# Kernel optimization log

Measured on AMD Instinct MI355X. Metric: run time of the kernel, lower is better.

The kernel has to match this reference:

```python
import jax, jax.numpy as jnp
import numpy as np

B, P, ENC = 128, 625, 512
A, E, H, V = 256, 256, 512, 70
START_TOK, END_TOK = 68, 69


def setup_inputs() -> dict:
    key = jax.random.key(0)
    ks = jax.random.split(key, 20)
    w = lambda k, shape: jax.random.normal(k, shape, jnp.float32) * 0.02
    return {
        "encoder_out": jax.random.normal(ks[0], (B, P, ENC), jnp.float32),
        "emb": w(ks[1], (V, E)),
        "We": w(ks[2], (ENC, A)), "be": jnp.zeros((A,), jnp.float32),
        "Wd": w(ks[3], (H, A)),   "bd": jnp.zeros((A,), jnp.float32),
        "wf": w(ks[4], (A,)),     "bf": jnp.zeros((), jnp.float32),
        "Wh0": w(ks[5], (ENC, H)), "bh0": jnp.zeros((H,), jnp.float32),
        "Wc0": w(ks[6], (ENC, H)), "bc0": jnp.zeros((H,), jnp.float32),
        "Wb": w(ks[7], (H, ENC)), "bb": jnp.zeros((ENC,), jnp.float32),
        "Wih": w(ks[8], (E + ENC, 4 * H)), "Whh": w(ks[9], (H, 4 * H)),
        "bih": jnp.zeros((4 * H,), jnp.float32), "bhh": jnp.zeros((4 * H,), jnp.float32),
        "Wfc": w(ks[10], (H, V)), "bfc": jnp.zeros((V,), jnp.float32),
        "decode_lengths": 70,
    }


def _decode(encoder_out, emb, We, be, Wd, bd, wf, bf, Wh0, bh0, Wc0, bc0,
            Wb, bb, Wih, Whh, bih, bhh, Wfc, bfc, decode_lengths):
    enc = encoder_out  # [B, P, ENC]
    batch = enc.shape[0]
    # encoder_att projection is constant across timesteps -> hoist out of loop
    att1 = enc @ We + be                      # [B, P, A]
    mean_enc = enc.mean(axis=1)               # [B, ENC]
    h0 = mean_enc @ Wh0 + bh0                 # [B, H]
    c0 = mean_enc @ Wc0 + bc0                 # [B, H]
    emb0 = emb[jnp.full((batch,), START_TOK)]  # [B, E]
    lstm_b = bih + bhh

    def step(carry, _):
        h, c, emb_t, done = carry
        att2 = h @ Wd + bd                                            # [B, A]
        e = jnp.einsum('bpa,a->bp', jax.nn.relu(att1 + att2[:, None, :]), wf) + bf
        alpha = jax.nn.softmax(e, axis=1)                             # [B, P]
        awe = jnp.einsum('bp,bpe->be', alpha, enc)                    # [B, ENC]
        awe = jax.nn.sigmoid(h @ Wb + bb) * awe                       # gated
        gates = jnp.concatenate([emb_t, awe], axis=1) @ Wih + h @ Whh + lstm_b
        i_, f_, g_, o_ = jnp.split(gates, 4, axis=1)                  # torch order i,f,g,o
        c_new = jax.nn.sigmoid(f_) * c + jax.nn.sigmoid(i_) * jnp.tanh(g_)
        h_new = jax.nn.sigmoid(o_) * jnp.tanh(c_new)
        preds = h_new @ Wfc + bfc                                     # [B, V] (dropout eval = id)
        preds_out = jnp.where(done, 0.0, preds)                       # zeros after early break
        done_new = done | (jnp.argmax(preds) == END_TOK)              # flat argmax, as in torch
        emb_new = emb[jnp.argmax(preds, axis=-1)]                     # greedy feedback
        return (h_new, c_new, emb_new, done_new), preds_out

    init = (h0, c0, emb0, jnp.array(False))
    _, preds_seq = jax.lax.scan(step, init, None, length=decode_lengths)
    return jnp.transpose(preds_seq, (1, 0, 2))  # [B, T, V]


def reference(encoder_out, emb, We, be, Wd, bd, wf, bf, Wh0, bh0, Wc0, bc0,
              Wb, bb, Wih, Whh, bih, bhh, Wfc, bfc, decode_lengths):
    return _decode(encoder_out, emb, We, be, Wd, bd, wf, bf, Wh0, bh0, Wc0, bc0,
                   Wb, bb, Wih, Whh, bih, bhh, Wfc, bfc, decode_lengths)
```

## Files before the change

### kernel.cpp

```cpp
#include <hip/hip_runtime.h>
#include <math.h>

#define Bn 128
#define Pn 625
#define ENCn 512
#define An 256
#define En 256
#define Hn 512
#define Vn 70
#define G4n 2048
#define STARTT 68
#define ENDT 69
#define NCHUNK 5
#define PCH 125
#define PSTRIDE 520
#define KSPLIT 16
#define KCH 80


__global__ __launch_bounds__(256) void k_mean(const float* __restrict__ enc,
                                              float* __restrict__ mean_enc) {
  int b = blockIdx.x, t = threadIdx.x;
  const float* e = enc + (size_t)b * Pn * ENCn;
  float s0 = 0.f, s1 = 0.f;
  for (int p = 0; p < Pn; ++p) {
    s0 += e[(size_t)p * ENCn + t];
    s1 += e[(size_t)p * ENCn + t + 256];
  }
  mean_enc[b * ENCn + t] = s0 * (1.0f / 625.0f);
  mean_enc[b * ENCn + t + 256] = s1 * (1.0f / 625.0f);
}

__global__ __launch_bounds__(512) void k_init(const float* __restrict__ mean_enc,
                       const float* __restrict__ Wh0, const float* __restrict__ bh0,
                       const float* __restrict__ Wc0, const float* __restrict__ bc0,
                       const float* __restrict__ emb,
                       float* __restrict__ h0, float* __restrict__ c0,
                       float* __restrict__ emb_t, int* __restrict__ done_arr) {
  int b = blockIdx.x, t = threadIdx.x;
  const float* W = blockIdx.y ? Wc0 : Wh0;
  const float* bias = blockIdx.y ? bc0 : bh0;
  float* out = blockIdx.y ? c0 : h0;
  __shared__ float ms[ENCn];
  ms[t] = mean_enc[b * ENCn + t];
  __syncthreads();
  float s = bias[t];
  for (int k = 0; k < ENCn; ++k) s += ms[k] * W[k * Hn + t];
  out[b * Hn + t] = s;
  if (blockIdx.y == 0 && t < En) emb_t[b * En + t] = emb[STARTT * En + t];
  if (blockIdx.y == 0 && b == 0 && t == 0) done_arr[0] = 0;
}

__global__ __launch_bounds__(256) void k_att1(const float* __restrict__ Am,
                       const float* __restrict__ We,
                       const float* __restrict__ be, float* __restrict__ att1) {
  __shared__ float sA[16][128];
  __shared__ float sB[16][128];
  int n0 = blockIdx.x * 128, m0 = blockIdx.y * 128;
  int t = threadIdx.x;
  int tm = (t >> 4) * 8, tn = (t & 15) * 8;
  float acc[8][8];
#pragma unroll
  for (int i = 0; i < 8; ++i)
#pragma unroll
    for (int j = 0; j < 8; ++j) acc[i][j] = 0.f;
  for (int k0 = 0; k0 < 512; k0 += 16) {
    __syncthreads();
#pragma unroll
    for (int i = 0; i < 8; ++i) {
      int idx = t + i * 256;
      int mm = idx >> 4, kk = idx & 15;
      sA[kk][mm] = Am[(size_t)(m0 + mm) * 512 + k0 + kk];
      int kk2 = idx >> 7, nn = idx & 127;
      sB[kk2][nn] = We[(size_t)(k0 + kk2) * 256 + n0 + nn];
    }
    __syncthreads();
#pragma unroll
    for (int kk = 0; kk < 16; ++kk) {
      float a[8], bq[8];
      *(float4*)&a[0] = *(const float4*)&sA[kk][tm];
      *(float4*)&a[4] = *(const float4*)&sA[kk][tm + 4];
      *(float4*)&bq[0] = *(const float4*)&sB[kk][tn];
      *(float4*)&bq[4] = *(const float4*)&sB[kk][tn + 4];
#pragma unroll
      for (int i = 0; i < 8; ++i)
#pragma unroll
        for (int j = 0; j < 8; ++j) acc[i][j] += a[i] * bq[j];
    }
  }
  float ber[8];
  *(float4*)&ber[0] = *(const float4*)&be[n0 + tn];
  *(float4*)&ber[4] = *(const float4*)&be[n0 + tn + 4];
#pragma unroll
  for (int i = 0; i < 8; ++i) {
    float o[8];
#pragma unroll
    for (int j = 0; j < 8; ++j) o[j] = acc[i][j] + ber[j];
    *(float4*)&att1[(size_t)(m0 + tm + i) * An + n0 + tn] = *(float4*)&o[0];
    *(float4*)&att1[(size_t)(m0 + tm + i) * An + n0 + tn + 4] = *(float4*)&o[4];
  }
}


__global__ __launch_bounds__(256) void k_proj(const float* __restrict__ h,
                       const float* __restrict__ Wd, const float* __restrict__ bd,
                       const float* __restrict__ Wb, const float* __restrict__ bbv,
                       float* __restrict__ att2, float* __restrict__ gate,
                       const float* __restrict__ preds,
                       const int* __restrict__ done_prev, int* __restrict__ done_cur,
                       int do_flat) {
  int t = threadIdx.x;
  if (blockIdx.x == Bn) {
    if (!do_flat) return;
    __shared__ float sv[256];
    __shared__ int si[256];
    float bv = -1e30f; int bi = 0x7fffffff;
    for (int i = t; i < Bn * Vn; i += 256) {
      float v = preds[i];
      if (v > bv) { bv = v; bi = i; }
    }
    sv[t] = bv; si[t] = bi;
    __syncthreads();
    for (int s = 128; s > 0; s >>= 1) {
      if (t < s) {
        if (sv[t + s] > sv[t] || (sv[t + s] == sv[t] && si[t + s] < si[t])) {
          sv[t] = sv[t + s]; si[t] = si[t + s];
        }
      }
      __syncthreads();
    }
    if (t == 0) *done_cur = (*done_prev) | (si[0] == ENDT ? 1 : 0);
    return;
  }
  int b = blockIdx.x;
  __shared__ float hsh[Hn];
  hsh[t] = h[b * Hn + t];
  hsh[t + 256] = h[b * Hn + t + 256];
  __syncthreads();
  float s0 = bd[t];
  float s1 = bbv[t], s2 = bbv[t + 256];
  for (int k = 0; k < Hn; ++k) {
    float hv = hsh[k];
    s0 += hv * Wd[(size_t)k * An + t];
    s1 += hv * Wb[(size_t)k * ENCn + t];
    s2 += hv * Wb[(size_t)k * ENCn + t + 256];
  }
  att2[b * An + t] = s0;
  gate[b * ENCn + t] = 1.f / (1.f + expf(-s1));
  gate[b * ENCn + t + 256] = 1.f / (1.f + expf(-s2));
}

__global__ __launch_bounds__(256) void k_attn(const float* __restrict__ att1,
                       const float* __restrict__ att2,
                       const float* __restrict__ wf, const float* __restrict__ bfp,
                       const float* __restrict__ enc, float* __restrict__ part) {
  int c = blockIdx.x, b = blockIdx.y, t = threadIdx.x;
  int lane = t & 63, wv = t >> 6;
  int p0 = c * PCH;
  __shared__ float es[PCH];
  __shared__ float red[256];
  float4 a2 = ((const float4*)(att2 + b * An))[lane];
  float4 wfr = ((const float4*)wf)[lane];
  float bfv = *bfp;
  const float* a1b = att1 + ((size_t)b * Pn + p0) * An;
  for (int p = wv; p < PCH; p += 4) {
    float4 v = ((const float4*)(a1b + (size_t)p * An))[lane];
    float s = fmaxf(v.x + a2.x, 0.f) * wfr.x
            + fmaxf(v.y + a2.y, 0.f) * wfr.y
            + fmaxf(v.z + a2.z, 0.f) * wfr.z
            + fmaxf(v.w + a2.w, 0.f) * wfr.w;
    for (int o = 32; o > 0; o >>= 1) s += __shfl_down(s, o, 64);
    if (lane == 0) es[p] = s + bfv;
  }
  __syncthreads();
  float m = -1e30f;
  for (int i = t; i < PCH; i += 256) m = fmaxf(m, es[i]);
  red[t] = m;
  __syncthreads();
  for (int s = 128; s > 0; s >>= 1) {
    if (t < s) red[t] = fmaxf(red[t], red[t + s]);
    __syncthreads();
  }
  m = red[0];
  __syncthreads();
  float lp = 0.f;
  for (int i = t; i < PCH; i += 256) {
    float e2 = expf(es[i] - m);
    es[i] = e2;
    lp += e2;
  }
  red[t] = lp;
  __syncthreads();
  for (int s = 128; s > 0; s >>= 1) {
    if (t < s) red[t] += red[t + s];
    __syncthreads();
  }
  float l = red[0];
  float acc0 = 0.f, acc1 = 0.f;
  const float* ebase = enc + ((size_t)b * Pn + p0) * ENCn;
  for (int p = 0; p < PCH; ++p) {
    float wp = es[p];
    acc0 += wp * ebase[(size_t)p * ENCn + t];
    acc1 += wp * ebase[(size_t)p * ENCn + t + 256];
  }
  float* pp = part + (size_t)(b * NCHUNK + c) * PSTRIDE;
  if (t == 0) { pp[0] = m; pp[1] = l; }
  pp[8 + t] = acc0;
  pp[8 + t + 256] = acc1;
}

__global__ __launch_bounds__(256) void k_combine(const float* __restrict__ part,
                       const float* __restrict__ gate, float* __restrict__ awe) {
  int b = blockIdx.x, t = threadIdx.x;
  const float* pb = part + (size_t)b * NCHUNK * PSTRIDE;
  float M = -1e30f;
#pragma unroll
  for (int c = 0; c < NCHUNK; ++c) M = fmaxf(M, pb[c * PSTRIDE]);
  float L = 0.f, sc[NCHUNK];
#pragma unroll
  for (int c = 0; c < NCHUNK; ++c) {
    float s = expf(pb[c * PSTRIDE] - M);
    sc[c] = s;
    L += s * pb[c * PSTRIDE + 1];
  }
  float inv = 1.f / L;
  float a0 = 0.f, a1 = 0.f;
#pragma unroll
  for (int c = 0; c < NCHUNK; ++c) {
    a0 += sc[c] * pb[c * PSTRIDE + 8 + t];
    a1 += sc[c] * pb[c * PSTRIDE + 8 + t + 256];
  }
  awe[b * ENCn + t] = a0 * inv * gate[b * ENCn + t];
  awe[b * ENCn + t + 256] = a1 * inv * gate[b * ENCn + t + 256];
}

__global__ __launch_bounds__(256) void k_gates(const float* __restrict__ embt,
                       const float* __restrict__ awe, const float* __restrict__ h,
                       const float* __restrict__ Wih, const float* __restrict__ Whh,
                       float* __restrict__ gp) {
  int n0 = blockIdx.x * 64;
  int sI = blockIdx.y;
  int k0 = sI * KCH;
  int t = threadIdx.x;
  int tc = t & 15, tg = t >> 4;
  int nc = n0 + tc * 4;
  float4 acc[8];
#pragma unroll
  for (int r = 0; r < 8; ++r) acc[r] = make_float4(0.f, 0.f, 0.f, 0.f);
  for (int kk = 0; kk < KCH; kk += 4) {
    int k = k0 + kk;
    const float* wbase = (k < 768) ? (Wih + (size_t)k * G4n + nc)
                                   : (Whh + (size_t)(k - 768) * G4n + nc);
    float4 w0 = *(const float4*)(wbase);
    float4 w1 = *(const float4*)(wbase + G4n);
    float4 w2 = *(const float4*)(wbase + 2 * G4n);
    float4 w3 = *(const float4*)(wbase + 3 * G4n);
#pragma unroll
    for (int r = 0; r < 8; ++r) {
      int row = tg * 8 + r;
      float4 xv;
      if (k < 256)      xv = *(const float4*)(embt + row * En + k);
      else if (k < 768) xv = *(const float4*)(awe + row * ENCn + (k - 256));
      else              xv = *(const float4*)(h + row * Hn + (k - 768));
      acc[r].x += xv.x * w0.x + xv.y * w1.x + xv.z * w2.x + xv.w * w3.x;
      acc[r].y += xv.x * w0.y + xv.y * w1.y + xv.z * w2.y + xv.w * w3.y;
      acc[r].z += xv.x * w0.z + xv.y * w1.z + xv.z * w2.z + xv.w * w3.z;
      acc[r].w += xv.x * w0.w + xv.y * w1.w + xv.z * w2.w + xv.w * w3.w;
    }
  }
#pragma unroll
  for (int r = 0; r < 8; ++r)
    *(float4*)(gp + ((size_t)sI * Bn + tg * 8 + r) * G4n + nc) = acc[r];
}

__global__ __launch_bounds__(512) void k_lstm(const float* __restrict__ gp,
                       const float* __restrict__ bih, const float* __restrict__ bhh,
                       const float* __restrict__ c_in, float* __restrict__ c_out,
                       float* __restrict__ h_out,
                       const float* __restrict__ Wfc, const float* __restrict__ bfc,
                       const float* __restrict__ emb, float* __restrict__ preds,
                       float* __restrict__ emb_next, float* __restrict__ out,
                       const int* __restrict__ done_t, int step, int T) {
  int b = blockIdx.x, t = threadIdx.x;
  float gi = bih[t] + bhh[t];
  float gf = bih[t + 512] + bhh[t + 512];
  float gg = bih[t + 1024] + bhh[t + 1024];
  float go = bih[t + 1536] + bhh[t + 1536];
  for (int s = 0; s < KSPLIT; ++s) {
    const float* row = gp + ((size_t)s * Bn + b) * G4n;
    gi += row[t];
    gf += row[t + 512];
    gg += row[t + 1024];
    go += row[t + 1536];
  }
  float cv = (1.f / (1.f + expf(-gf))) * c_in[b * Hn + t]
           + (1.f / (1.f + expf(-gi))) * tanhf(gg);
  float hv = (1.f / (1.f + expf(-go))) * tanhf(cv);
  c_out[b * Hn + t] = cv;
  h_out[b * Hn + t] = hv;
  __shared__ float hs[Hn];
  __shared__ float ps[Vn];
  __shared__ int tokS;
  hs[t] = hv;
  __syncthreads();
  int lane = t & 63, wvi = t >> 6;
  for (int v = wvi; v < Vn; v += 8) {
    float s = 0.f;
    for (int k = lane; k < Hn; k += 64) s += hs[k] * Wfc[(size_t)k * Vn + v];
    for (int o = 32; o > 0; o >>= 1) s += __shfl_down(s, o, 64);
    if (lane == 0) ps[v] = s + bfc[v];
  }
  __syncthreads();
  int done = *done_t;
  if (t < Vn) {
    float pv = ps[t];
    preds[b * Vn + t] = pv;
    out[((size_t)b * T + step) * Vn + t] = done ? 0.f : pv;
  }
  if (t == 0) {
    float bv = ps[0]; int bi = 0;
    for (int v = 1; v < Vn; ++v)
      if (ps[v] > bv) { bv = ps[v]; bi = v; }
    tokS = bi;
  }
  __syncthreads();
  if (t < En) emb_next[b * En + t] = emb[tokS * En + t];
}


extern "C" void kernel_launch(void* const* d_in, const int* in_sizes, int n_in,
                              void* d_out, int out_size, void* d_ws, size_t ws_size,
                              hipStream_t stream) {
  const float* enc = (const float*)d_in[0];
  const float* emb = (const float*)d_in[1];
  const float* We  = (const float*)d_in[2];
  const float* be  = (const float*)d_in[3];
  const float* Wd  = (const float*)d_in[4];
  const float* bd  = (const float*)d_in[5];
  const float* wf  = (const float*)d_in[6];
  const float* bf  = (const float*)d_in[7];
  const float* Wh0 = (const float*)d_in[8];
  const float* bh0 = (const float*)d_in[9];
  const float* Wc0 = (const float*)d_in[10];
  const float* bc0 = (const float*)d_in[11];
  const float* Wb  = (const float*)d_in[12];
  const float* bb  = (const float*)d_in[13];
  const float* Wih = (const float*)d_in[14];
  const float* Whh = (const float*)d_in[15];
  const float* bih = (const float*)d_in[16];
  const float* bhh = (const float*)d_in[17];
  const float* Wfc = (const float*)d_in[18];
  const float* bfc = (const float*)d_in[19];
  int T = out_size / (Bn * Vn);

  float* w = (float*)d_ws;
  size_t off = 0;
  float* att1 = w + off;     off += (size_t)Bn * Pn * An;
  float* mean_enc = w + off; off += Bn * ENCn;
  float* hb0 = w + off;      off += Bn * Hn;
  float* hb1 = w + off;      off += Bn * Hn;
  float* cb0 = w + off;      off += Bn * Hn;
  float* cb1 = w + off;      off += Bn * Hn;
  float* eb0 = w + off;      off += Bn * En;
  float* eb1 = w + off;      off += Bn * En;
  float* att2 = w + off;     off += Bn * An;
  float* gate = w + off;     off += Bn * ENCn;
  float* part = w + off;     off += (size_t)Bn * NCHUNK * PSTRIDE;
  float* awe = w + off;      off += Bn * ENCn;
  float* gatesP = w + off;   off += (size_t)KSPLIT * Bn * G4n;
  float* preds = w + off;    off += Bn * Vn;
  off = (off + 255) & ~(size_t)255;
  int* done_arr = (int*)(w + off);

  float* hbuf[2] = {hb0, hb1};
  float* cbuf[2] = {cb0, cb1};
  float* ebuf[2] = {eb0, eb1};

  k_mean<<<Bn, 256, 0, stream>>>(enc, mean_enc);
  k_init<<<dim3(Bn, 2), 512, 0, stream>>>(mean_enc, Wh0, bh0, Wc0, bc0, emb,
                                          hb0, cb0, eb0, done_arr);
  k_att1<<<dim3(2, 625), 256, 0, stream>>>(enc, We, be, att1);

  int cur = 0;
  for (int t = 0; t < T; ++t) {
    int nxt = cur ^ 1;
    k_proj<<<Bn + 1, 256, 0, stream>>>(hbuf[cur], Wd, bd, Wb, bb, att2, gate, preds,
                                       done_arr + (t > 0 ? t - 1 : 0), done_arr + t,
                                       t > 0 ? 1 : 0);
    k_attn<<<dim3(NCHUNK, Bn), 256, 0, stream>>>(att1, att2, wf, bf, enc, part);
    k_combine<<<Bn, 256, 0, stream>>>(part, gate, awe);
    k_gates<<<dim3(32, KSPLIT), 256, 0, stream>>>(ebuf[cur], awe, hbuf[cur], Wih, Whh, gatesP);
    k_lstm<<<Bn, 512, 0, stream>>>(gatesP, bih, bhh, cbuf[cur], cbuf[nxt], hbuf[nxt],
                                   Wfc, bfc, emb, preds, ebuf[nxt], (float*)d_out,
                                   done_arr + t, t, T);
    cur = nxt;
  }
}
```

Measured before the change: 10.05 ms.

## Split proj kernel across columns, transpose Wfc, vectorize attention, halve gate K-split

The per-step projection kernel is split across a 3-wide grid so the Wd and Wb halves run in separate blocks, giving three times as many blocks and fewer dependent loads per thread. Wfc is transposed once up front so the LSTM output projection reads contiguous memory per wavefront. The attention-weighted sum now uses float2 loads and stores with unrolling. The gate GEMM K-split drops from 16 to 8, with a longer K range per block, which shrinks the partial-sum traffic read back by the LSTM kernel but gives fewer blocks. The costs are one extra setup kernel, a small workspace buffer, and possibly lower occupancy in the gates kernel.

After: 10.66 ms. +6.1%, slower.

```diff
diff --git a/kernel.cpp b/kernel.cpp
--- a/kernel.cpp
+++ b/kernel.cpp
@@ -14,8 +14,8 @@
 #define NCHUNK 5
 #define PCH 125
 #define PSTRIDE 520
-#define KSPLIT 16
-#define KCH 80
+#define KSPLIT 8
+#define KCH 160
 
 
 __global__ __launch_bounds__(256) void k_mean(const float* __restrict__ enc,
@@ -29,6 +29,15 @@
   }
   mean_enc[b * ENCn + t] = s0 * (1.0f / 625.0f);
   mean_enc[b * ENCn + t + 256] = s1 * (1.0f / 625.0f);
+}
+
+__global__ __launch_bounds__(256) void k_prep(const float* __restrict__ Wfc,
+                                              float* __restrict__ WfcT) {
+  int j = blockIdx.x * 256 + threadIdx.x;
+  if (j < Hn * Vn) {
+    int k = j / Vn, vv = j - k * Vn;
+    WfcT[(size_t)vv * Hn + k] = Wfc[j];
+  }
 }
 
 __global__ __launch_bounds__(512) void k_init(const float* __restrict__ mean_enc,
@@ -111,7 +120,7 @@
                        int do_flat) {
   int t = threadIdx.x;
   if (blockIdx.x == Bn) {
-    if (!do_flat) return;
+    if (blockIdx.y != 0 || !do_flat) return;
     __shared__ float sv[256];
     __shared__ int si[256];
     float bv = -1e30f; int bi = 0x7fffffff;
@@ -132,22 +141,23 @@
     if (t == 0) *done_cur = (*done_prev) | (si[0] == ENDT ? 1 : 0);
     return;
   }
-  int b = blockIdx.x;
+  int b = blockIdx.x, g = blockIdx.y;
   __shared__ float hsh[Hn];
   hsh[t] = h[b * Hn + t];
   hsh[t + 256] = h[b * Hn + t + 256];
   __syncthreads();
-  float s0 = bd[t];
-  float s1 = bbv[t], s2 = bbv[t + 256];
-  for (int k = 0; k < Hn; ++k) {
-    float hv = hsh[k];
-    s0 += hv * Wd[(size_t)k * An + t];
-    s1 += hv * Wb[(size_t)k * ENCn + t];
-    s2 += hv * Wb[(size_t)k * ENCn + t + 256];
-  }
-  att2[b * An + t] = s0;
-  gate[b * ENCn + t] = 1.f / (1.f + expf(-s1));
-  gate[b * ENCn + t + 256] = 1.f / (1.f + expf(-s2));
+  if (g == 0) {
+    float s = bd[t];
+#pragma unroll 8
+    for (int k = 0; k < Hn; ++k) s += hsh[k] * Wd[(size_t)k * An + t];
+    att2[b * An + t] = s;
+  } else {
+    int col = (g - 1) * 256 + t;
+    float s = bbv[col];
+#pragma unroll 8
+    for (int k = 0; k < Hn; ++k) s += hsh[k] * Wb[(size_t)k * ENCn + col];
+    gate[b * ENCn + col] = 1.f / (1.f + expf(-s));
+  }
 }
 
 __global__ __launch_bounds__(256) void k_attn(const float* __restrict__ att1,
@@ -198,15 +208,16 @@
   float l = red[0];
   float acc0 = 0.f, acc1 = 0.f;
   const float* ebase = enc + ((size_t)b * Pn + p0) * ENCn;
+#pragma unroll 4
   for (int p = 0; p < PCH; ++p) {
     float wp = es[p];
-    acc0 += wp * ebase[(size_t)p * ENCn + t];
-    acc1 += wp * ebase[(size_t)p * ENCn + t + 256];
+    float2 ev = ((const float2*)(ebase + (size_t)p * ENCn))[t];
+    acc0 += wp * ev.x;
+    acc1 += wp * ev.y;
   }
   float* pp = part + (size_t)(b * NCHUNK + c) * PSTRIDE;
   if (t == 0) { pp[0] = m; pp[1] = l; }
-  pp[8 + t] = acc0;
-  pp[8 + t + 256] = acc1;
+  *(float2*)&pp[8 + 2 * t] = make_float2(acc0, acc1);
 }
 
 __global__ __launch_bounds__(256) void k_combine(const float* __restrict__ part,
@@ -277,7 +288,7 @@
                        const float* __restrict__ bih, const float* __restrict__ bhh,
                        const float* __restrict__ c_in, float* __restrict__ c_out,
                        float* __restrict__ h_out,
-                       const float* __restrict__ Wfc, const float* __restrict__ bfc,
+                       const float* __restrict__ WfcT, const float* __restrict__ bfc,
                        const float* __restrict__ emb, float* __restrict__ preds,
                        float* __restrict__ emb_next, float* __restrict__ out,
                        const int* __restrict__ done_t, int step, int T) {
@@ -306,7 +317,7 @@
   int lane = t & 63, wvi = t >> 6;
   for (int v = wvi; v < Vn; v += 8) {
     float s = 0.f;
-    for (int k = lane; k < Hn; k += 64) s += hs[k] * Wfc[(size_t)k * Vn + v];
+    for (int k = lane; k < Hn; k += 64) s += hs[k] * WfcT[(size_t)v * Hn + k];
     for (int o = 32; o > 0; o >>= 1) s += __shfl_down(s, o, 64);
     if (lane == 0) ps[v] = s + bfc[v];
   }
@@ -356,6 +367,7 @@
   float* w = (float*)d_ws;
   size_t off = 0;
   float* att1 = w + off;     off += (size_t)Bn * Pn * An;
+  float* WfcT = w + off;     off += (size_t)Hn * Vn;
   float* mean_enc = w + off; off += Bn * ENCn;
   float* hb0 = w + off;      off += Bn * Hn;
   float* hb1 = w + off;      off += Bn * Hn;
@@ -377,6 +389,7 @@
   float* ebuf[2] = {eb0, eb1};
 
   k_mean<<<Bn, 256, 0, stream>>>(enc, mean_enc);
+  k_prep<<<(Hn * Vn + 255) / 256, 256, 0, stream>>>(Wfc, WfcT);
   k_init<<<dim3(Bn, 2), 512, 0, stream>>>(mean_enc, Wh0, bh0, Wc0, bc0, emb,
                                           hb0, cb0, eb0, done_arr);
   k_att1<<<dim3(2, 625), 256, 0, stream>>>(enc, We, be, att1);
@@ -384,14 +397,14 @@
   int cur = 0;
   for (int t = 0; t < T; ++t) {
     int nxt = cur ^ 1;
-    k_proj<<<Bn + 1, 256, 0, stream>>>(hbuf[cur], Wd, bd, Wb, bb, att2, gate, preds,
+    k_proj<<<dim3(Bn + 1, 3), 256, 0, stream>>>(hbuf[cur], Wd, bd, Wb, bb, att2, gate, preds,
                                        done_arr + (t > 0 ? t - 1 : 0), done_arr + t,
                                        t > 0 ? 1 : 0);
     k_attn<<<dim3(NCHUNK, Bn), 256, 0, stream>>>(att1, att2, wf, bf, enc, part);
     k_combine<<<Bn, 256, 0, stream>>>(part, gate, awe);
     k_gates<<<dim3(32, KSPLIT), 256, 0, stream>>>(ebuf[cur], awe, hbuf[cur], Wih, Whh, gatesP);
     k_lstm<<<Bn, 512, 0, stream>>>(gatesP, bih, bhh, cbuf[cur], cbuf[nxt], hbuf[nxt],
-                                   Wfc, bfc, emb, preds, ebuf[nxt], (float*)d_out,
+                                   WfcT, bfc, emb, preds, ebuf[nxt], (float*)d_out,
                                    done_arr + t, t, T);
     cur = nxt;
   }
```
